# Kernel optimization log

Measured on AMD Instinct MI355X. Metric: run time of the kernel, lower is better.

## Reference

```python
import jax, jax.numpy as jnp
import numpy as np

N, E = 10000, 80000
IN_C, HID, HEADS = 128, 256, 8
NEG_SLOPE = 0.2


def setup_inputs() -> dict:
    key = jax.random.key(0)
    ks = jax.random.split(key, 16)
    s = lambda k, shape, fan: jax.random.normal(k, shape, jnp.float32) * (1.0 / np.sqrt(fan))
    return {
        "x": jax.random.normal(ks[0], (N, IN_C), jnp.float32),
        "edge_index": jax.random.randint(ks[1], (2, E), 0, N, jnp.int64),
        "edge_weight": jax.random.uniform(ks[2], (E,), jnp.float32),
        # GATConv params
        "W_gat": s(ks[3], (IN_C, HEADS * HID), IN_C),
        "att_src": s(ks[4], (HEADS, HID), HID),
        "att_dst": s(ks[5], (HEADS, HID), HID),
        "b_gat": jnp.zeros((HEADS * HID,), jnp.float32),
        # SAGEConv params (lin_l on aggregated neighbors, lin_r on root)
        "W_sage_l": s(ks[6], (HEADS * HID, HID), HEADS * HID),
        "b_sage_l": jnp.zeros((HID,), jnp.float32),
        "W_sage_r": s(ks[7], (HEADS * HID, HID), HEADS * HID),
        # MLP head
        "W_lin1": s(ks[8], (HID, HID // 2), HID),
        "b_lin1": jnp.zeros((HID // 2,), jnp.float32),
        "W_lin2": s(ks[9], (HID // 2, 1), HID // 2),
        "b_lin2": jnp.zeros((1,), jnp.float32),
    }


def reference(x, edge_index, edge_weight, W_gat, att_src, att_dst, b_gat,
              W_sage_l, b_sage_l, W_sage_r, W_lin1, b_lin1, W_lin2, b_lin2):
    n = x.shape[0]
    src, dst = edge_index[0], edge_index[1]

    # ---- GATConv (edge_attr ignored since edge_dim=None in PyG) ----
    h = (x @ W_gat).reshape(n, HEADS, HID)            # [N,H,C]
    a_src = jnp.sum(h * att_src, axis=-1)             # [N,H]
    a_dst = jnp.sum(h * att_dst, axis=-1)             # [N,H]
    e = a_src[src] + a_dst[dst]                       # [E,H]
    e = jax.nn.leaky_relu(e, NEG_SLOPE)
    # segment softmax over edges sharing a destination node
    e_max = jax.ops.segment_max(e, dst, num_segments=n)   # [N,H]
    e_exp = jnp.exp(e - e_max[dst])                        # [E,H]
    denom = jax.ops.segment_sum(e_exp, dst, num_segments=n)
    alpha = e_exp / (denom[dst] + 1e-16)                   # [E,H]
    msg = h[src] * alpha[:, :, None]                       # [E,H,C]
    out1 = jax.ops.segment_sum(msg, dst, num_segments=n).reshape(n, HEADS * HID) + b_gat
    x1 = jax.nn.relu(out1)                                 # [N, H*C]; dropout is identity at inference

    # ---- SAGEConv (mean aggregation) ----
    deg = jax.ops.segment_sum(jnp.ones((src.shape[0],), x1.dtype), dst, num_segments=n)
    agg = jax.ops.segment_sum(x1[src], dst, num_segments=n) / jnp.maximum(deg, 1.0)[:, None]
    x2 = jax.nn.relu(agg @ W_sage_l + b_sage_l + x1 @ W_sage_r)  # [N, HID]

    # ---- MLP head ----
    hmid = jax.nn.relu(x2 @ W_lin1 + b_lin1)
    return hmid @ W_lin2 + b_lin2                           # [N,1]
```

## Files before the change

kernel.cpp:

```cpp
#include <hip/hip_runtime.h>
#include <math.h>

#define HEADS 8
#define HID 256
#define INC 128
#define GDIM 2048
#define NEG_SLOPE 0.2f

typedef unsigned short ushort_t;
typedef short bf16x8 __attribute__((ext_vector_type(8)));
typedef ushort_t u16x8 __attribute__((ext_vector_type(8)));
typedef float f32x4 __attribute__((ext_vector_type(4)));

__device__ __forceinline__ ushort_t f2bf(float f) {
  union { float f; unsigned u; } v; v.f = f;
  unsigned r = (v.u + 0x7FFF + ((v.u >> 16) & 1)) >> 16;
  return (ushort_t)r;
}
__device__ __forceinline__ float bf2f(ushort_t u) {
  union { unsigned u; float f; } v; v.u = ((unsigned)u) << 16;
  return v.f;
}

__device__ __forceinline__ void gload_lds16(const ushort_t* g, ushort_t* l) {
  __builtin_amdgcn_global_load_lds(
      (const __attribute__((address_space(1))) unsigned int*)g,
      (__attribute__((address_space(3))) unsigned int*)l, 16, 0, 0);
}

__device__ __forceinline__ int src_chunk(int lane) {
  return ((lane & 3) - ((lane >> 3) & 3)) & 3;
}
__device__ __forceinline__ int rd_chunk(int lc, int kg) {
  return (kg + ((lc >> 1) & 3)) & 3;
}

__global__ __launch_bounds__(256) void prep(
    const float* __restrict__ x, ushort_t* __restrict__ xb,
    const float* __restrict__ Wg, ushort_t* __restrict__ WgT,
    const float* __restrict__ Wl, const float* __restrict__ Wr, ushort_t* __restrict__ WsT,
    const int* __restrict__ ei, int* __restrict__ deg, int E,
    const float* __restrict__ att_s, const float* __restrict__ att_d, float* __restrict__ wt,
    int o1, int o2, int o3, int o4, int o5)
{
  __shared__ float tile[32][33];
  __shared__ float attl[256];
  int b = blockIdx.x, t = threadIdx.x;
  if (b < o1) {
    int i = b * 1024 + t * 4;
    float4 v = *(const float4*)(x + i);
    ushort_t o[4] = {f2bf(v.x), f2bf(v.y), f2bf(v.z), f2bf(v.w)};
    *(unsigned long long*)(xb + i) = *(unsigned long long*)o;
  } else if (b < o4) {
    const float* src; ushort_t* dst; int R, C, rowOff, bx, by;
    if (b < o2)      { int idx = b - o1; src = Wg; dst = WgT; R = INC;  C = GDIM; rowOff = 0;   bx = idx % (INC / 32);  by = idx / (INC / 32); }
    else if (b < o3) { int idx = b - o2; src = Wl; dst = WsT; R = GDIM; C = HID;  rowOff = 0;   bx = idx % (GDIM / 32); by = idx / (GDIM / 32); }
    else             { int idx = b - o3; src = Wr; dst = WsT; R = GDIM; C = HID;  rowOff = HID; bx = idx % (GDIM / 32); by = idx / (GDIM / 32); }
    int tx = t & 31, ty = t >> 5;
    int r0 = bx * 32, c0 = by * 32;
    #pragma unroll
    for (int i = 0; i < 32; i += 8)
      tile[ty + i][tx] = src[(size_t)(r0 + ty + i) * C + c0 + tx];
    __syncthreads();
    #pragma unroll
    for (int i = 0; i < 32; i += 8)
      dst[(size_t)(rowOff + c0 + ty + i) * R + r0 + tx] = f2bf(tile[tx][ty + i]);
  } else if (b < o5) {
    int e = (b - o4) * 256 + t;
    if (e < E) atomicAdd(&deg[ei[E + e]], 1);
  } else {
    int j = b - o5;
    int hd = j & 7;
    const float* att = (j < 8) ? att_s : att_d;
    if (t < 256) attl[t] = att[hd * 256 + t];
    __syncthreads();
    if (t < 128) {
      float acc = 0.f;
      #pragma unroll 8
      for (int c = 0; c < 256; ++c)
        acc += Wg[(size_t)t * GDIM + hd * 256 + c] * attl[c];
      wt[j * 128 + t] = acc;
    }
  }
}

__global__ __launch_bounds__(256) void a_dots(
    const ushort_t* __restrict__ xb, const float* __restrict__ wt,
    float* __restrict__ a_all, int N)
{
  __shared__ float wts[16][132];
  __shared__ ushort_t xs[16 * 128];
  int t = threadIdx.x;
  for (int i = t; i < 2048; i += 256) wts[i >> 7][i & 127] = wt[i];
  int b0 = blockIdx.x * 16;
  {
    int row = t >> 4, off = (t & 15) * 8;
    int n = b0 + row; if (n >= N) n = N - 1;
    *(u16x8*)&xs[row * 128 + off] = *(const u16x8*)(xb + (size_t)n * 128 + off);
  }
  __syncthreads();
  int nl = t >> 4, j = t & 15;
  float acc = 0.f;
  #pragma unroll 8
  for (int k = 0; k < 128; ++k)
    acc += bf2f(xs[nl * 128 + k]) * wts[j][k];
  int n = b0 + nl;
  if (n < N) a_all[(size_t)n * 16 + j] = acc;
}

__global__ __launch_bounds__(1024) void scan_deg(const int* __restrict__ deg, int* __restrict__ start,
                                                 int* __restrict__ cursor, int N)
{
  __shared__ int sums[1024];
  int t = threadIdx.x;
  int chunk = (N + 1023) / 1024;
  int s = 0;
  for (int i = 0; i < chunk; ++i) {
    int idx = t * chunk + i;
    if (idx < N) s += deg[idx];
  }
  sums[t] = s;
  __syncthreads();
  for (int off = 1; off < 1024; off <<= 1) {
    int v = (t >= off) ? sums[t - off] : 0;
    __syncthreads();
    sums[t] += v;
    __syncthreads();
  }
  int run = (t == 0) ? 0 : sums[t - 1];
  for (int i = 0; i < chunk; ++i) {
    int idx = t * chunk + i;
    if (idx < N) { start[idx] = run; cursor[idx] = run; run += deg[idx]; }
  }
}

__global__ void fill_buckets(const int* __restrict__ ei, int* __restrict__ cursor,
                             int* __restrict__ srcs, int E)
{
  int e = blockIdx.x * 256 + threadIdx.x;
  if (e < E) {
    int n = ei[E + e];
    int p = atomicAdd(&cursor[n], 1);
    srcs[p] = ei[e];
  }
}

__global__ __launch_bounds__(256) void gat_aggregate(
    const ushort_t* __restrict__ xb, const float* __restrict__ a_all,
    const int* __restrict__ start, const int* __restrict__ deg,
    const int* __restrict__ srcs, ushort_t* __restrict__ aggb, int N)
{
  int n = blockIdx.x, t = threadIdx.x;
  __shared__ float adst[8];
  __shared__ float emax[8];
  __shared__ float esum[8];
  __shared__ float red[256];
  __shared__ float alpha_s[32][8];
  __shared__ int src_s[32];
  int cnt = deg[n];
  int base = start[n];
  if (t < 8) adst[t] = a_all[(size_t)n * 16 + 8 + t];
  __syncthreads();
  int hd = t & 7, lj = t >> 3;
  float m = -1e30f;
  for (int j = lj; j < cnt; j += 32) {
    int s = srcs[base + j];
    float v = a_all[(size_t)s * 16 + hd] + adst[hd];
    v = v > 0.f ? v : NEG_SLOPE * v;
    m = fmaxf(m, v);
  }
  red[t] = m;
  __syncthreads();
  #pragma unroll
  for (int off = 128; off >= 8; off >>= 1) {
    if (t < off) red[t] = fmaxf(red[t], red[t + off]);
    __syncthreads();
  }
  if (t < 8) emax[t] = red[t];
  __syncthreads();
  float ssum = 0.f;
  for (int j = lj; j < cnt; j += 32) {
    int s = srcs[base + j];
    float v = a_all[(size_t)s * 16 + hd] + adst[hd];
    v = v > 0.f ? v : NEG_SLOPE * v;
    ssum += expf(v - emax[hd]);
  }
  red[t] = ssum;
  __syncthreads();
  #pragma unroll
  for (int off = 128; off >= 8; off >>= 1) {
    if (t < off) red[t] += red[t + off];
    __syncthreads();
  }
  if (t < 8) esum[t] = red[t] + 1e-16f;
  __syncthreads();
  int d = t & 127, hg = t >> 7;
  float acc[4] = {0.f, 0.f, 0.f, 0.f};
  for (int j0 = 0; j0 < cnt; j0 += 32) {
    int j = j0 + lj;
    if (j < cnt) {
      int s = srcs[base + j];
      if (hd == 0) src_s[lj] = s;
      float v = a_all[(size_t)s * 16 + hd] + adst[hd];
      v = v > 0.f ? v : NEG_SLOPE * v;
      alpha_s[lj][hd] = expf(v - emax[hd]) / esum[hd];
    }
    __syncthreads();
    int lim = cnt - j0; if (lim > 32) lim = 32;
    for (int el = 0; el < lim; ++el) {
      float v = bf2f(xb[(size_t)src_s[el] * INC + d]);
      #pragma unroll
      for (int k = 0; k < 4; ++k) acc[k] += v * alpha_s[el][hg * 4 + k];
    }
    __syncthreads();
  }
  #pragma unroll
  for (int k = 0; k < 4; ++k)
    aggb[(size_t)n * 1024 + (hg * 4 + k) * INC + d] = f2bf(acc[k]);
}

__global__ __launch_bounds__(256) void gemm_gat(
    const ushort_t* __restrict__ A, const ushort_t* __restrict__ BT,
    const float* __restrict__ b_gat, ushort_t* __restrict__ x1, int M)
{
  __shared__ ushort_t As[2][128][32];
  __shared__ ushort_t Bs[2][128][32];
  int tid = threadIdx.x;
  int wave = tid >> 6, lane = tid & 63;
  int row0 = blockIdx.x * 128;
  int head = blockIdx.y >> 1, colblk = blockIdx.y & 1;
  const ushort_t* Abase = A + head * INC;
  const ushort_t* Bbase = BT + ((size_t)head * 256 + colblk * 128) * INC;
  int wr = (wave >> 1) * 64, wc = (wave & 1) * 64;
  int lc = lane & 15, kg = lane >> 4;
  int sc = src_chunk(lane), srow = lane >> 2;

  f32x4 acc[4][4] = {};

  #define STAGE_G(buf, kt)                                                        \
    _Pragma("unroll")                                                             \
    for (int c = 0; c < 2; ++c) {                                                 \
      int r = c * 64 + wave * 16 + srow;                                          \
      int ga = row0 + r; if (ga >= M) ga = M - 1;                                 \
      gload_lds16(Abase + (size_t)ga * 1024 + (kt) + sc * 8, &As[buf][c * 64 + wave * 16][0]); \
      gload_lds16(Bbase + (size_t)r * INC + (kt) + sc * 8, &Bs[buf][c * 64 + wave * 16][0]); \
    }

  #define COMPUTE_G(buf)                                                          \
    {                                                                             \
      bf16x8 af[4], bfr[4];                                                       \
      _Pragma("unroll")                                                           \
      for (int mi = 0; mi < 4; ++mi)                                              \
        af[mi] = *(const bf16x8*)&As[buf][wr + mi * 16 + lc][rd_chunk(lc, kg) * 8]; \
      _Pragma("unroll")                                                           \
      for (int ni = 0; ni < 4; ++ni)                                              \
        bfr[ni] = *(const bf16x8*)&Bs[buf][wc + ni * 16 + lc][rd_chunk(lc, kg) * 8]; \
      _Pragma("unroll")                                                           \
      for (int mi = 0; mi < 4; ++mi)                                              \
        _Pragma("unroll")                                                         \
        for (int ni = 0; ni < 4; ++ni)                                            \
          acc[mi][ni] = __builtin_amdgcn_mfma_f32_16x16x32_bf16(af[mi], bfr[ni], acc[mi][ni], 0, 0, 0); \
    }

  STAGE_G(0, 0);
  __syncthreads();
  int cur = 0;
  for (int kt = 32; kt < INC; kt += 32) {
    STAGE_G(cur ^ 1, kt);
    COMPUTE_G(cur);
    __syncthreads();
    cur ^= 1;
  }
  COMPUTE_G(cur);
  #undef STAGE_G
  #undef COMPUTE_G

  int gcol0 = head * 256 + colblk * 128;
  float bg[4];
  #pragma unroll
  for (int ni = 0; ni < 4; ++ni) bg[ni] = b_gat[gcol0 + wc + ni * 16 + lc];
  #pragma unroll
  for (int mi = 0; mi < 4; ++mi) {
    #pragma unroll
    for (int r = 0; r < 4; ++r) {
      int grow = row0 + wr + mi * 16 + kg * 4 + r;
      if (grow < M) {
        #pragma unroll
        for (int ni = 0; ni < 4; ++ni) {
          float v = acc[mi][ni][r] + bg[ni];
          x1[(size_t)grow * GDIM + gcol0 + wc + ni * 16 + lc] = f2bf(v > 0.f ? v : 0.f);
        }
      }
    }
  }
}

__global__ __launch_bounds__(512) void gemm_sage(
    const ushort_t* __restrict__ A, const ushort_t* __restrict__ BT,
    ushort_t* __restrict__ C, int M, int Nc, int K)
{
  __shared__ ushort_t As[2][64][32];
  __shared__ ushort_t Bs[2][256][32];
  int tid = threadIdx.x;
  int wave = tid >> 6, lane = tid & 63;
  int row0 = blockIdx.x * 64, col0 = blockIdx.y * 256;
  int wr = (wave >> 2) * 32, wc = (wave & 3) * 64;
  int lc = lane & 15, kg = lane >> 4;
  int sc = src_chunk(lane), srow = lane >> 2;

  f32x4 acc[2][4] = {};

  #define STAGE_S(buf, kt)                                                        \
    {                                                                             \
      if (wave < 4) {                                                             \
        int ga = row0 + wave * 16 + srow; if (ga >= M) ga = M - 1;                \
        gload_lds16(A + (size_t)ga * K + (kt) + sc * 8, &As[buf][wave * 16][0]);  \
      }                                                                           \
      _Pragma("unroll")                                                           \
      for (int c = 0; c < 2; ++c) {                                               \
        int gb = col0 + c * 128 + wave * 16 + srow;                               \
        gload_lds16(BT + (size_t)gb * K + (kt) + sc * 8, &Bs[buf][c * 128 + wave * 16][0]); \
      }                                                                           \
    }

  #define COMPUTE_S(buf)                                                          \
    {                                                                             \
      bf16x8 af[2], bfr[4];                                                       \
      _Pragma("unroll")                                                           \
      for (int mi = 0; mi < 2; ++mi)                                              \
        af[mi] = *(const bf16x8*)&As[buf][wr + mi * 16 + lc][rd_chunk(lc, kg) * 8]; \
      _Pragma("unroll")                                                           \
      for (int ni = 0; ni < 4; ++ni)                                              \
        bfr[ni] = *(const bf16x8*)&Bs[buf][wc + ni * 16 + lc][rd_chunk(lc, kg) * 8]; \
      _Pragma("unroll")                                                           \
      for (int mi = 0; mi < 2; ++mi)                                              \
        _Pragma("unroll")                                                         \
        for (int ni = 0; ni < 4; ++ni)                                            \
          acc[mi][ni] = __builtin_amdgcn_mfma_f32_16x16x32_bf16(af[mi], bfr[ni], acc[mi][ni], 0, 0, 0); \
    }

  STAGE_S(0, 0);
  __syncthreads();
  int cur = 0;
  for (int kt = 32; kt < K; kt += 32) {
    STAGE_S(cur ^ 1, kt);
    COMPUTE_S(cur);
    __syncthreads();
    cur ^= 1;
  }
  COMPUTE_S(cur);
  #undef STAGE_S
  #undef COMPUTE_S

  #pragma unroll
  for (int mi = 0; mi < 2; ++mi) {
    #pragma unroll
    for (int r = 0; r < 4; ++r) {
      int grow = row0 + wr + mi * 16 + kg * 4 + r;
      if (grow < M) {
        #pragma unroll
        for (int ni = 0; ni < 4; ++ni)
          C[(size_t)grow * Nc + col0 + wc + ni * 16 + lc] = f2bf(acc[mi][ni][r]);
      }
    }
  }
}

__global__ __launch_bounds__(256) void sage_mlp(
    const ushort_t* __restrict__ yb, const int* __restrict__ start, const int* __restrict__ deg,
    const int* __restrict__ srcs, const float* __restrict__ b_l,
    const float* __restrict__ W1, const float* __restrict__ b1,
    const float* __restrict__ W2, const float* __restrict__ b2, float* __restrict__ out, int N)
{
  __shared__ float xs[16][256];
  __shared__ float wred[4][8];
  int t = threadIdx.x;
  int wv = t >> 6, lane = t & 63;
  int b0 = blockIdx.x * 16;

  int half = lane >> 5;
  int col32 = lane & 31;
  for (int i = 0; i < 4; ++i) {
    int nl = wv * 4 + i;
    int n = b0 + nl;
    float acc[8] = {0.f, 0.f, 0.f, 0.f, 0.f, 0.f, 0.f, 0.f};
    if (n < N) {
      int cnt = deg[n];
      int base = start[n];
      for (int j = 0; j < cnt; j += 2) {
        int jj = j + half;
        if (jj < cnt) {
          int s = srcs[base + jj];
          u16x8 v = *(const u16x8*)(yb + (size_t)s * 512 + col32 * 8);
          #pragma unroll
          for (int k = 0; k < 8; ++k) acc[k] += bf2f(v[k]);
        }
      }
      #pragma unroll
      for (int k = 0; k < 8; ++k) acc[k] += __shfl_xor(acc[k], 32);
      if (half == 0) {
        float d = (float)cnt; if (d < 1.f) d = 1.f;
        u16x8 r = *(const u16x8*)(yb + (size_t)n * 512 + 256 + col32 * 8);
        #pragma unroll
        for (int k = 0; k < 8; ++k) {
          float v = acc[k] / d + bf2f(r[k]) + b_l[col32 * 8 + k];
          xs[nl][col32 * 8 + k] = v > 0.f ? v : 0.f;
        }
      }
    } else if (half == 0) {
      #pragma unroll
      for (int k = 0; k < 8; ++k) xs[nl][col32 * 8 + k] = 0.f;
    }
  }
  __syncthreads();

  int c = t & 127, g = t >> 7;
  float acc[8];
  float bb = b1[c];
  #pragma unroll
  for (int nn = 0; nn < 8; ++nn) acc[nn] = bb;
  for (int k = 0; k < 256; ++k) {
    float w = W1[k * 128 + c];
    #pragma unroll
    for (int nn = 0; nn < 8; ++nn) acc[nn] += xs[g * 8 + nn][k] * w;
  }
  float w2 = W2[c];
  float p[8];
  #pragma unroll
  for (int nn = 0; nn < 8; ++nn) {
    float hm = acc[nn] > 0.f ? acc[nn] : 0.f;
    p[nn] = hm * w2;
  }
  #pragma unroll
  for (int off = 32; off >= 1; off >>= 1)
    #pragma unroll
    for (int nn = 0; nn < 8; ++nn) p[nn] += __shfl_down(p[nn], off);
  if ((t & 63) == 0) {
    #pragma unroll
    for (int nn = 0; nn < 8; ++nn) wred[wv][nn] = p[nn];
  }
  __syncthreads();
  if (t < 16) {
    int gg = t >> 3, nn = t & 7;
    int node = b0 + gg * 8 + nn;
    if (node < N)
      out[node] = wred[gg * 2][nn] + wred[gg * 2 + 1][nn] + b2[0];
  }
}

extern "C" void kernel_launch(void* const* d_in, const int* in_sizes, int n_in,
                              void* d_out, int out_size, void* d_ws, size_t ws_size,
                              hipStream_t stream)
{
  const float* x        = (const float*)d_in[0];
  const int*   ei       = (const int*)d_in[1];
  const float* W_gat    = (const float*)d_in[3];
  const float* att_src  = (const float*)d_in[4];
  const float* att_dst  = (const float*)d_in[5];
  const float* b_gat    = (const float*)d_in[6];
  const float* W_sage_l = (const float*)d_in[7];
  const float* b_sage_l = (const float*)d_in[8];
  const float* W_sage_r = (const float*)d_in[9];
  const float* W_lin1   = (const float*)d_in[10];
  const float* b_lin1   = (const float*)d_in[11];
  const float* W_lin2   = (const float*)d_in[12];
  const float* b_lin2   = (const float*)d_in[13];
  float* out = (float*)d_out;

  const int N = in_sizes[0] / INC;
  const int E = in_sizes[1] / 2;

  char* p = (char*)d_ws;
  ushort_t* x1b   = (ushort_t*)p;         p += (size_t)N * GDIM * 2;
  ushort_t* aggb  = (ushort_t*)p;         p += (size_t)N * 1024 * 2;
  ushort_t* yb    = (ushort_t*)p;         p += (size_t)N * 512 * 2;
  ushort_t* xb    = (ushort_t*)p;         p += (size_t)N * INC * 2;
  ushort_t* WgatT = (ushort_t*)p;         p += (size_t)GDIM * INC * 2;
  ushort_t* WsT   = (ushort_t*)p;         p += (size_t)512 * GDIM * 2;
  float*    wt    = (float*)p;            p += (size_t)16 * 128 * 4;
  float*    a_all = (float*)p;            p += (size_t)N * 16 * 4;
  int*      deg   = (int*)p;              p += (size_t)N * 4;
  int*      start = (int*)p;              p += (size_t)N * 4;
  int*      cursor= (int*)p;              p += (size_t)N * 4;
  int*      srcs  = (int*)p;              p += (size_t)E * 4;

  hipMemsetAsync(deg, 0, (size_t)N * sizeof(int), stream);

  int nbX   = (N * INC + 1023) / 1024;
  int nbWg  = (INC / 32) * (GDIM / 32);
  int nbWs  = (GDIM / 32) * (HID / 32);
  int nbDeg = (E + 255) / 256;
  int o1 = nbX, o2 = o1 + nbWg, o3 = o2 + nbWs, o4 = o3 + nbWs, o5 = o4 + nbDeg;
  int nbTot = o5 + 16;
  prep<<<nbTot, 256, 0, stream>>>(x, xb, W_gat, WgatT, W_sage_l, W_sage_r, WsT,
                                  ei, deg, E, att_src, att_dst, wt, o1, o2, o3, o4, o5);

  scan_deg<<<1, 1024, 0, stream>>>(deg, start, cursor, N);
  fill_buckets<<<(E + 255) / 256, 256, 0, stream>>>(ei, cursor, srcs, E);

  a_dots<<<(N + 15) / 16, 256, 0, stream>>>(xb, wt, a_all, N);

  gat_aggregate<<<N, 256, 0, stream>>>(xb, a_all, start, deg, srcs, aggb, N);

  { dim3 grid((N + 127) / 128, 16);
    gemm_gat<<<grid, 256, 0, stream>>>(aggb, WgatT, b_gat, x1b, N); }

  { dim3 grid((N + 63) / 64, 512 / 256);
    gemm_sage<<<grid, 512, 0, stream>>>(x1b, WsT, yb, N, 512, GDIM); }

  sage_mlp<<<(N + 15) / 16, 256, 0, stream>>>(yb, start, deg, srcs, b_sage_l,
                                              W_lin1, b_lin1, W_lin2, b_lin2, out, N);
}
```

Baseline: 181.0 us.

## Split-K the SAGE GEMM into four partials and add a reduction kernel

The SAGE GEMM (K=2048) is split along K into four slices via a third grid dimension, each writing bf16 partial results to a new workspace buffer. A separate kernel sums the four partials into the final output. The aim is to raise parallelism and occupancy for a GEMM whose grid was only about 314 blocks. The cost is an extra launch, roughly four times the output write and read traffic, and extra bf16 rounding on the partial sums.

```diff
diff --git a/kernel.cpp b/kernel.cpp
--- a/kernel.cpp
+++ b/kernel.cpp
@@ -6,6 +6,7 @@
 #define INC 128
 #define GDIM 2048
 #define NEG_SLOPE 0.2f
+#define KSPLIT 4
 
 typedef unsigned short ushort_t;
 typedef short bf16x8 __attribute__((ext_vector_type(8)));
@@ -297,13 +298,15 @@
 
 __global__ __launch_bounds__(512) void gemm_sage(
     const ushort_t* __restrict__ A, const ushort_t* __restrict__ BT,
-    ushort_t* __restrict__ C, int M, int Nc, int K)
+    ushort_t* __restrict__ Cp, int M, int Nc, int K, int Klen)
 {
   __shared__ ushort_t As[2][64][32];
   __shared__ ushort_t Bs[2][256][32];
   int tid = threadIdx.x;
   int wave = tid >> 6, lane = tid & 63;
   int row0 = blockIdx.x * 64, col0 = blockIdx.y * 256;
+  int k0 = blockIdx.z * Klen;
+  ushort_t* C = Cp + (size_t)blockIdx.z * M * Nc;
   int wr = (wave >> 2) * 32, wc = (wave & 3) * 64;
   int lc = lane & 15, kg = lane >> 4;
   int sc = src_chunk(lane), srow = lane >> 2;
@@ -339,10 +342,10 @@
           acc[mi][ni] = __builtin_amdgcn_mfma_f32_16x16x32_bf16(af[mi], bfr[ni], acc[mi][ni], 0, 0, 0); \
     }
 
-  STAGE_S(0, 0);
+  STAGE_S(0, k0);
   __syncthreads();
   int cur = 0;
-  for (int kt = 32; kt < K; kt += 32) {
+  for (int kt = k0 + 32; kt < k0 + Klen; kt += 32) {
     STAGE_S(cur ^ 1, kt);
     COMPUTE_S(cur);
     __syncthreads();
@@ -364,6 +367,25 @@
       }
     }
   }
+}
+
+__global__ __launch_bounds__(256) void yreduce(
+    const ushort_t* __restrict__ yp, ushort_t* __restrict__ yb, size_t stride, int total8)
+{
+  int i = blockIdx.x * 256 + threadIdx.x;
+  if (i >= total8) return;
+  size_t off = (size_t)i * 8;
+  float s[8] = {0.f, 0.f, 0.f, 0.f, 0.f, 0.f, 0.f, 0.f};
+  #pragma unroll
+  for (int z = 0; z < KSPLIT; ++z) {
+    u16x8 v = *(const u16x8*)(yp + z * stride + off);
+    #pragma unroll
+    for (int k = 0; k < 8; ++k) s[k] += bf2f(v[k]);
+  }
+  u16x8 o;
+  #pragma unroll
+  for (int k = 0; k < 8; ++k) o[k] = f2bf(s[k]);
+  *(u16x8*)(yb + off) = o;
 }
 
 __global__ __launch_bounds__(256) void sage_mlp(
@@ -473,6 +495,7 @@
   char* p = (char*)d_ws;
   ushort_t* x1b   = (ushort_t*)p;         p += (size_t)N * GDIM * 2;
   ushort_t* aggb  = (ushort_t*)p;         p += (size_t)N * 1024 * 2;
+  ushort_t* ypart = (ushort_t*)p;         p += (size_t)KSPLIT * N * 512 * 2;
   ushort_t* yb    = (ushort_t*)p;         p += (size_t)N * 512 * 2;
   ushort_t* xb    = (ushort_t*)p;         p += (size_t)N * INC * 2;
   ushort_t* WgatT = (ushort_t*)p;         p += (size_t)GDIM * INC * 2;
@@ -505,8 +528,10 @@
   { dim3 grid((N + 127) / 128, 16);
     gemm_gat<<<grid, 256, 0, stream>>>(aggb, WgatT, b_gat, x1b, N); }
 
-  { dim3 grid((N + 63) / 64, 512 / 256);
-    gemm_sage<<<grid, 512, 0, stream>>>(x1b, WsT, yb, N, 512, GDIM); }
+  { dim3 grid((N + 63) / 64, 512 / 256, KSPLIT);
+    gemm_sage<<<grid, 512, 0, stream>>>(x1b, WsT, ypart, N, 512, GDIM, GDIM / KSPLIT); }
+  { int total8 = N * 512 / 8;
+    yreduce<<<(total8 + 255) / 256, 256, 0, stream>>>(ypart, yb, (size_t)N * 512, total8); }
 
   sage_mlp<<<(N + 15) / 16, 256, 0, stream>>>(yb, start, deg, srcs, b_sage_l,
                                               W_lin1, b_lin1, W_lin2, b_lin2, out, N);
```

New measurement: 180.7 us. No clear change (-0.2%).
